# Performance work log

Measured on AMD Instinct MI355X. Metric: run time of the kernel, lower is better.

Reference implementation:

```python
import jax, jax.numpy as jnp
import numpy as np
from jax import lax

B, S, D, V, MAXLEN = 32, 2048, 1024, 32000, 2048
EPS = jnp.finfo(jnp.float32).eps  # torch RMSNorm default eps=None -> finfo eps


def setup_inputs() -> dict:
    key = jax.random.key(0)
    ks = jax.random.split(key, 10)
    w = lambda k, shape: (jax.random.normal(k, shape, jnp.float32) * 0.02)
    return {
        "x": jax.random.randint(ks[0], (B, S), 0, V),
        "emb": w(ks[1], (V, D)),
        "pos": w(ks[2], (MAXLEN, D)),
        "conv_w": w(ks[3], (3, D, D)),            # HIO layout (k, in, out)
        "conv_b": jnp.zeros((D,), jnp.float32),
        "wg1": w(ks[4], (D, D)), "bg1": jnp.zeros((D,), jnp.float32),
        "wmv": w(ks[5], (2 * D, D)), "bmv": jnp.zeros((D,), jnp.float32),
        "wmg": w(ks[6], (2 * D, D)), "bmg": jnp.zeros((D,), jnp.float32),
        "wrg": w(ks[7], (2 * D, D)), "brg": jnp.zeros((D,), jnp.float32),
        "rms_w": jnp.ones((D,), jnp.float32),
        "wp": w(ks[8], (2 * D, V)), "bp": jnp.zeros((V,), jnp.float32),
    }


def _rmsnorm(v, rms_w):
    ms = jnp.mean(v * v, axis=-1, keepdims=True)
    return v * lax.rsqrt(ms + EPS) * rms_w


def reference(x, emb, pos, conv_w, conv_b, wg1, bg1, wmv, bmv, wmg, bmg,
              wrg, brg, rms_w, wp, bp):
    seq_len = x.shape[1]
    h = emb[x] + pos[:seq_len]                     # [B, S, D]
    # Conv1d(D, D, k=3, padding=1) over the sequence axis
    h = lax.conv_general_dilated(h, conv_w, window_strides=(1,),
                                 padding=((1, 1),),
                                 dimension_numbers=("NHC", "HIO", "NHC")) + conv_b
    nodes = h * jax.nn.sigmoid(h @ wg1 + bg1)      # gated nodes [B, S, D]

    curr = nodes[:, :-1, :]                        # nodes_past [B, S-1, D]
    while curr.shape[1] > 1:                       # log2(S) static levels
        if curr.shape[1] % 2 != 0:
            curr = jnp.concatenate([curr, curr[:, -1:, :]], axis=1)
        left = curr[:, 0::2, :]
        right = curr[:, 1::2, :]
        combined = jnp.concatenate([left, right], axis=-1)   # [B, n/2, 2D]
        val = combined @ wmv + bmv
        gate = jax.nn.sigmoid(combined @ wmg + bmg)
        merged = _rmsnorm(val * gate, rms_w)
        res_gate = jax.nn.sigmoid(combined @ wrg + brg)
        residual = (left + right) * 0.5
        curr = res_gate * merged + (1.0 - res_gate) * residual

    root = curr[:, 0, :]                           # [B, D]
    last = nodes[:, -2, :]                         # last of nodes_past
    context = jnp.concatenate([root, last], axis=-1)  # [B, 2D]
    return context @ wp + bp                       # logits [B, V]
```

## Files before the change

### kernel.cpp

```cpp
#include <hip/hip_runtime.h>
#include <stdint.h>

typedef __bf16 bf16_t;
typedef __attribute__((ext_vector_type(8))) __bf16 bf16x8;
typedef __attribute__((ext_vector_type(4))) __bf16 bf16x4;
typedef __attribute__((ext_vector_type(4))) float f32x4;

#define NB 32
#define NS 2048
#define ND 1024
#define NV 32000
#define SP 2050

__device__ __forceinline__ float sigmoid_(float x) { return 1.0f / (1.0f + __expf(-x)); }

__device__ __forceinline__ void gload_lds16(const void* g, void* lds) {
  __builtin_amdgcn_global_load_lds((const __attribute__((address_space(1))) void*)g,
                                   (__attribute__((address_space(3))) void*)lds, 16, 0, 0);
}


__global__ void zero_pad_k(bf16_t* h0p) {
  int i = blockIdx.x;
  int b = i >> 1;
  size_t row = (size_t)b * SP + ((i & 1) ? (SP - 1) : 0);
  bf16x4 z = {};
  *(bf16x4*)(h0p + row * ND + threadIdx.x * 4) = z;
}

__global__ void embed_k(const int* __restrict__ x, const float* __restrict__ emb,
                        const float* __restrict__ pos, bf16_t* __restrict__ h0p) {
  int bs = blockIdx.x;
  int b = bs >> 11, s = bs & (NS - 1);
  int idx = x[bs];
  const float* e = emb + (size_t)idx * ND;
  const float* p = pos + (size_t)s * ND;
  bf16_t* o = h0p + ((size_t)b * SP + s + 1) * ND;
  int d = threadIdx.x * 4;
  f32x4 ev = *(const f32x4*)(e + d);
  f32x4 pv = *(const f32x4*)(p + d);
  bf16x4 ov;
  ov[0] = (bf16_t)(ev[0] + pv[0]);
  ov[1] = (bf16_t)(ev[1] + pv[1]);
  ov[2] = (bf16_t)(ev[2] + pv[2]);
  ov[3] = (bf16_t)(ev[3] + pv[3]);
  *(bf16x4*)(o + d) = ov;
}

__global__ void conv_transpose_k(const float* __restrict__ in, bf16_t* __restrict__ out,
                                 int R, int C) {
  __shared__ float tile[32][33];
  int tc = blockIdx.x * 32, tr = blockIdx.y * 32;
  int tx = threadIdx.x;
  for (int i = threadIdx.y; i < 32; i += 8)
    tile[i][tx] = in[(size_t)(tr + i) * C + tc + tx];
  __syncthreads();
  for (int i = threadIdx.y; i < 32; i += 8)
    out[(size_t)(tc + i) * R + tr + tx] = (bf16_t)tile[tx][i];
}

__global__ void dup_row_k(bf16_t* nodes) {
  int b = blockIdx.x;
  const bf16_t* src = nodes + ((size_t)b * NS + NS - 2) * ND;
  bf16_t* dst = nodes + ((size_t)b * NS + NS - 1) * ND;
  int d = threadIdx.x * 4;
  *(bf16x4*)(dst + d) = *(const bf16x4*)(src + d);
}

__global__ void concat3_k(const float* __restrict__ a, const float* __restrict__ b,
                          const float* __restrict__ c, float* __restrict__ o) {
  int i = blockIdx.x * 256 + threadIdx.x;
  o[i] = i < 1024 ? a[i] : (i < 2048 ? b[i - 1024] : c[i - 2048]);
}

template <int EPI>
__global__ __launch_bounds__(512, 2) void gemm256(
    const bf16_t* __restrict__ A, const bf16_t* __restrict__ Bt,
    const float* __restrict__ bias, const void* aux, void* Cout,
    int M, int N, int K, int lda, int batchShift, int batchPad,
    int GX, int gpx, int nxg, int ych) {
  const int tid = threadIdx.x;
  const int lane = tid & 63;
  const int wave = tid >> 6;
  int n0, m0;
  if (nxg == 0) {
    n0 = (blockIdx.x % GX) * 256;
    m0 = (blockIdx.x / GX) * 256;
  } else {
    const int id = blockIdx.x;
    const int xcd = id & 7;
    const int jb = id >> 3;
    const int xg = xcd % nxg;
    const int ysub = xcd / nxg;
    n0 = (xg * gpx + (jb % gpx)) * 256;
    m0 = (ysub * ych + (jb / gpx)) * 256;
  }
  const int waveM = wave >> 2, waveN = wave & 3;

  __shared__ __align__(16) bf16_t sA[2][256 * 64];
  __shared__ __align__(16) bf16_t sB[2][256 * 64];

  f32x4 acc[8][4] = {};

  const int srow = tid >> 3;
  const int sj = tid & 7;
  const int wbase = wave * 8;

  auto stageA = [&](int buf, int kt, int half) {
#pragma unroll
    for (int r = 0; r < 2; ++r) {
      int lr = half * 128 + r * 64 + srow;
      int sc = sj ^ (lr & 7);
      int g = m0 + lr;
      if (g > M - 1) g = M - 1;
      size_t grow = (size_t)g + (size_t)(((unsigned)g) >> batchShift) * batchPad;
      gload_lds16(A + grow * (size_t)lda + (kt * 64 + sc * 8),
                  &sA[buf][(size_t)(half * 128 + r * 64 + wbase) * 64]);
    }
  };
  auto stageB = [&](int buf, int kt, int half) {
#pragma unroll
    for (int r = 0; r < 2; ++r) {
      int lr = half * 128 + r * 64 + srow;
      int sc = sj ^ (lr & 7);
      int g = n0 + lr;
      if (g > N - 1) g = N - 1;
      gload_lds16(Bt + (size_t)g * K + (kt * 64 + sc * 8),
                  &sB[buf][(size_t)(half * 128 + r * 64 + wbase) * 64]);
    }
  };

  const int nt = K >> 6;
  stageA(0, 0, 0); stageA(0, 0, 1);
  stageB(0, 0, 0); stageB(0, 0, 1);
  if (nt > 1) {
    stageB(1, 1, 0); stageB(1, 1, 1);
    asm volatile("s_waitcnt vmcnt(4)" ::: "memory");
  } else {
    asm volatile("s_waitcnt vmcnt(0)" ::: "memory");
  }
  __builtin_amdgcn_s_barrier();

  const int rlane = lane & 15;
  const int klane = lane >> 4;
  bf16x8 bfr[4][2];

  for (int t = 0; t < nt; ++t) {
    const int buf = t & 1;
    const bf16_t* sa = sA[buf];
    const bf16_t* sb = sB[buf];
#pragma unroll
    for (int p = 0; p < 4; ++p) {
      if (p == 0) {
#pragma unroll
        for (int j = 0; j < 4; ++j)
#pragma unroll
          for (int ks = 0; ks < 2; ++ks) {
            int rb = waveN * 64 + j * 16 + rlane;
            int kc = ks * 4 + klane;
            bfr[j][ks] = *(const bf16x8*)&sb[rb * 64 + ((kc ^ (rb & 7)) * 8)];
          }
      }
      bf16x8 af[2][2];
#pragma unroll
      for (int ii = 0; ii < 2; ++ii)
#pragma unroll
        for (int ks = 0; ks < 2; ++ks) {
          int ra = waveM * 128 + p * 32 + ii * 16 + rlane;
          int kc = ks * 4 + klane;
          af[ii][ks] = *(const bf16x8*)&sa[ra * 64 + ((kc ^ (ra & 7)) * 8)];
        }
      if (p == 0) {
        if (t + 1 < nt) { stageA(buf ^ 1, t + 1, 0); stageA(buf ^ 1, t + 1, 1); }
      } else if (p == 1) {
        if (t + 2 < nt) stageB(buf, t + 2, 0);
      } else if (p == 2) {
        if (t + 2 < nt) stageB(buf, t + 2, 1);
      }
      __builtin_amdgcn_s_barrier();
      __builtin_amdgcn_s_setprio(1);
#pragma unroll
      for (int ks = 0; ks < 2; ++ks)
#pragma unroll
        for (int ii = 0; ii < 2; ++ii)
#pragma unroll
          for (int j = 0; j < 4; ++j)
            acc[p * 2 + ii][j] = __builtin_amdgcn_mfma_f32_16x16x32_bf16(
                af[ii][ks], bfr[j][ks], acc[p * 2 + ii][j], 0, 0, 0);
      __builtin_amdgcn_s_setprio(0);
      if (p < 3) {
        __builtin_amdgcn_s_barrier();
      } else {
        if (t + 2 < nt)
          asm volatile("s_waitcnt vmcnt(4)" ::: "memory");
        else
          asm volatile("s_waitcnt vmcnt(0)" ::: "memory");
        __builtin_amdgcn_s_barrier();
      }
    }
  }

  const int colBase = n0 + waveN * 64 + rlane;
#pragma unroll
  for (int i = 0; i < 8; ++i) {
    const int rowBase = m0 + waveM * 128 + i * 16 + klane * 4;
#pragma unroll
    for (int j = 0; j < 4; ++j) {
      const int col = colBase + j * 16;
      const float bv = bias[col];
#pragma unroll
      for (int r = 0; r < 4; ++r) {
        const int row = rowBase + r;
        if (row >= M) continue;
        float v = acc[i][j][r] + bv;
        size_t o = (size_t)row * N + col;
        if constexpr (EPI == 0) {
          ((bf16_t*)Cout)[o] = (bf16_t)v;
        } else if constexpr (EPI == 1) {
          float hh = (float)((const bf16_t*)aux)[o];
          ((bf16_t*)Cout)[o] = (bf16_t)(hh * sigmoid_(v));
        } else {
          ((bf16_t*)Cout)[o] = (bf16_t)(col < 1024 ? v : sigmoid_(v));
        }
      }
    }
  }
}

template <bool ATOMIC>
__global__ __launch_bounds__(256, 2) void gemm128s(
    const bf16_t* __restrict__ A, const bf16_t* __restrict__ Bt,
    const float* __restrict__ bias, float* __restrict__ Cout,
    int M, int kLen, int nxy) {
  const int tid = threadIdx.x;
  const int lane = tid & 63;
  const int wave = tid >> 6;
  const int id = blockIdx.x;
  const int sk = id / nxy;
  const int rb2 = id % nxy;
  const int n0 = (rb2 % 24) * 128;
  const int m0 = (rb2 / 24) * 128;
  const int kOff = sk * kLen;

  const int waveM = wave >> 1, waveN = wave & 1;

  __shared__ __align__(16) bf16_t sA[2][128 * 64];
  __shared__ __align__(16) bf16_t sB[2][128 * 64];

  f32x4 acc[4][4] = {};

  const int srow = wave * 8 + (lane >> 3);
  const int sj = lane & 7;

  auto stage = [&](int buf, int kk0) {
#pragma unroll
    for (int j = 0; j < 4; ++j) {
      int rowT = j * 32 + srow;
      int k8 = sj ^ (rowT & 7);
      int gm = m0 + rowT;
      if (gm > M - 1) gm = M - 1;
      gload_lds16(A + (size_t)gm * 2048 + (kk0 + k8 * 8), &sA[buf][(j * 256 + wave * 64) * 8]);
      int gn = n0 + rowT;
      gload_lds16(Bt + (size_t)gn * 2048 + (kk0 + k8 * 8), &sB[buf][(j * 256 + wave * 64) * 8]);
    }
  };

  stage(0, kOff);
  __syncthreads();

  const int nt = kLen >> 6;
  int cur = 0;
  const int ar = waveM * 64 + (lane & 15);
  const int br = waveN * 64 + (lane & 15);
  const int kb0 = lane >> 4;

  for (int t = 0; t < nt; ++t) {
    if (t + 1 < nt) stage(cur ^ 1, kOff + (t + 1) * 64);

    const bf16_t* sa = sA[cur];
    const bf16_t* sb = sB[cur];
    bf16x8 af[2][4], bfr[2][4];
#pragma unroll
    for (int ks = 0; ks < 2; ++ks) {
      int kb = kb0 + ks * 4;
#pragma unroll
      for (int i = 0; i < 4; ++i) {
        int ra = ar + i * 16;
        af[ks][i] = *(const bf16x8*)&sa[ra * 64 + ((kb ^ (ra & 7)) * 8)];
        int rbq = br + i * 16;
        bfr[ks][i] = *(const bf16x8*)&sb[rbq * 64 + ((kb ^ (rbq & 7)) * 8)];
      }
    }
#pragma unroll
    for (int ks = 0; ks < 2; ++ks)
#pragma unroll
      for (int i = 0; i < 4; ++i)
#pragma unroll
        for (int j = 0; j < 4; ++j)
          acc[i][j] = __builtin_amdgcn_mfma_f32_16x16x32_bf16(af[ks][i], bfr[ks][j], acc[i][j], 0, 0, 0);
    __syncthreads();
    cur ^= 1;
  }

  const int colBase = n0 + waveN * 64 + (lane & 15);
#pragma unroll
  for (int i = 0; i < 4; ++i) {
    const int rowBase = m0 + waveM * 64 + i * 16 + (lane >> 4) * 4;
#pragma unroll
    for (int jj = 0; jj < 4; ++jj) {
      const int col = colBase + jj * 16;
      const float bv = (!ATOMIC || kOff == 0) ? bias[col] : 0.0f;
#pragma unroll
      for (int r = 0; r < 4; ++r) {
        const int row = rowBase + r;
        if (row >= M) continue;
        float v = acc[i][jj][r] + bv;
        size_t o = (size_t)row * 3072 + col;
        if constexpr (ATOMIC)
          atomicAdd(&Cout[o], v);
        else
          Cout[o] = v;
      }
    }
  }
}

__global__ __launch_bounds__(256) void tree_combine_k(
    const bf16_t* __restrict__ fb, const bf16_t* __restrict__ cur,
    const float* __restrict__ rms_w, bf16_t* __restrict__ outb) {
  const int m = blockIdx.x;
  const int t = threadIdx.x;
  const int d = t * 4;
  const bf16_t* row = fb + (size_t)m * 3072;
  bf16x4 vb = *(const bf16x4*)(row + d);
  bf16x4 gb = *(const bf16x4*)(row + 1024 + d);
  bf16x4 rb = *(const bf16x4*)(row + 2048 + d);
  f32x4 vg;
#pragma unroll
  for (int k = 0; k < 4; ++k) vg[k] = (float)vb[k] * (float)gb[k];
  float ss = vg[0] * vg[0] + vg[1] * vg[1] + vg[2] * vg[2] + vg[3] * vg[3];
#pragma unroll
  for (int o = 32; o > 0; o >>= 1) ss += __shfl_xor(ss, o);
  __shared__ float red[4];
  if ((t & 63) == 0) red[t >> 6] = ss;
  __syncthreads();
  float ms = (red[0] + red[1] + red[2] + red[3]) * (1.0f / ND);
  float scale = rsqrtf(ms + 1.1920929e-07f);
  f32x4 w = *(const f32x4*)(rms_w + d);
  const bf16_t* c0 = cur + (size_t)m * 2048;
  bf16x4 lv = *(const bf16x4*)(c0 + d);
  bf16x4 rv = *(const bf16x4*)(c0 + ND + d);
  bf16x4 o4;
#pragma unroll
  for (int k = 0; k < 4; ++k) {
    float merged = vg[k] * scale * w[k];
    float resid = 0.5f * ((float)lv[k] + (float)rv[k]);
    float g = (float)rb[k];
    o4[k] = (bf16_t)(g * merged + (1.0f - g) * resid);
  }
  *(bf16x4*)(outb + (size_t)m * ND + d) = o4;
}

__global__ __launch_bounds__(256) void tree_combine32_k(
    const float* __restrict__ fb, const bf16_t* __restrict__ cur,
    const float* __restrict__ rms_w, bf16_t* __restrict__ outb) {
  const int m = blockIdx.x;
  const int t = threadIdx.x;
  const int d = t * 4;
  const float* row = fb + (size_t)m * 3072;
  f32x4 v = *(const f32x4*)(row + d);
  f32x4 gl = *(const f32x4*)(row + 1024 + d);
  f32x4 rl = *(const f32x4*)(row + 2048 + d);
  f32x4 vg;
#pragma unroll
  for (int k = 0; k < 4; ++k) vg[k] = v[k] * sigmoid_(gl[k]);
  float ss = vg[0] * vg[0] + vg[1] * vg[1] + vg[2] * vg[2] + vg[3] * vg[3];
#pragma unroll
  for (int o = 32; o > 0; o >>= 1) ss += __shfl_xor(ss, o);
  __shared__ float red[4];
  if ((t & 63) == 0) red[t >> 6] = ss;
  __syncthreads();
  float ms = (red[0] + red[1] + red[2] + red[3]) * (1.0f / ND);
  float scale = rsqrtf(ms + 1.1920929e-07f);
  f32x4 w = *(const f32x4*)(rms_w + d);
  const bf16_t* c0 = cur + (size_t)m * 2048;
  bf16x4 lv = *(const bf16x4*)(c0 + d);
  bf16x4 rv = *(const bf16x4*)(c0 + ND + d);
  bf16x4 o4;
#pragma unroll
  for (int k = 0; k < 4; ++k) {
    float merged = vg[k] * scale * w[k];
    float resid = 0.5f * ((float)lv[k] + (float)rv[k]);
    float g = sigmoid_(rl[k]);
    o4[k] = (bf16_t)(g * merged + (1.0f - g) * resid);
  }
  *(bf16x4*)(outb + (size_t)m * ND + d) = o4;
}

__global__ void build_ctx_k(const bf16_t* __restrict__ root, const bf16_t* __restrict__ nodes,
                            float* __restrict__ ctx) {
  int b = blockIdx.x, t = threadIdx.x;
  const bf16_t* r = root + (size_t)b * ND;
  const bf16_t* l = nodes + ((size_t)b * NS + NS - 2) * ND;
  int d = t * 4;
#pragma unroll
  for (int k = 0; k < 4; ++k) {
    ctx[(size_t)b * 2048 + d + k] = (float)r[d + k];
    ctx[(size_t)b * 2048 + ND + d + k] = (float)l[d + k];
  }
}

__global__ __launch_bounds__(256) void final_proj_k(
    const float* __restrict__ ctx, const float* __restrict__ wp,
    const float* __restrict__ bp, float* __restrict__ out) {
  const int v = blockIdx.x * 256 + threadIdx.x;
  float acc[NB];
#pragma unroll
  for (int b = 0; b < NB; ++b) acc[b] = 0.f;
  __shared__ float sctx[NB][128];
  for (int k0 = 0; k0 < 2048; k0 += 128) {
    __syncthreads();
    for (int i = threadIdx.x; i < NB * 128; i += 256) {
      int bb = i >> 7, kk = i & 127;
      sctx[bb][kk] = ctx[(size_t)bb * 2048 + k0 + kk];
    }
    __syncthreads();
    for (int kk = 0; kk < 128; ++kk) {
      float wv = wp[(size_t)(k0 + kk) * NV + v];
#pragma unroll
      for (int b = 0; b < NB; ++b) acc[b] += sctx[b][kk] * wv;
    }
  }
#pragma unroll
  for (int b = 0; b < NB; ++b) out[(size_t)b * NV + v] = acc[b] + bp[v];
}

extern "C" void kernel_launch(void* const* d_in, const int* in_sizes, int n_in,
                              void* d_out, int out_size, void* d_ws, size_t ws_size,
                              hipStream_t stream) {
  const int* x = (const int*)d_in[0];
  const float* emb = (const float*)d_in[1];
  const float* pos = (const float*)d_in[2];
  const float* conv_w = (const float*)d_in[3];
  const float* conv_b = (const float*)d_in[4];
  const float* wg1 = (const float*)d_in[5];
  const float* bg1 = (const float*)d_in[6];
  const float* wmv = (const float*)d_in[7];
  const float* bmv = (const float*)d_in[8];
  const float* wmg = (const float*)d_in[9];
  const float* bmg = (const float*)d_in[10];
  const float* wrg = (const float*)d_in[11];
  const float* brg = (const float*)d_in[12];
  const float* rms_w = (const float*)d_in[13];
  const float* wp = (const float*)d_in[14];
  const float* bp = (const float*)d_in[15];
  float* out = (float*)d_out;

  char* ws = (char*)d_ws;
  size_t off = 0;
  auto alloc = [&](size_t bytes) -> void* {
    void* p = ws + off;
    off += (bytes + 255) & ~(size_t)255;
    return p;
  };
  bf16_t* h0p = (bf16_t*)alloc((size_t)NB * SP * ND * 2);
  bf16_t* h = (bf16_t*)alloc((size_t)NB * NS * ND * 2);
  bf16_t* nodes = (bf16_t*)alloc((size_t)NB * NS * ND * 2);
  bf16_t* tb0 = (bf16_t*)alloc((size_t)NB * 1024 * ND * 2);
  bf16_t* tb1 = (bf16_t*)alloc((size_t)NB * 1024 * ND * 2);
  bf16_t* convT = (bf16_t*)alloc((size_t)ND * 3072 * 2);
  bf16_t* wg1T = (bf16_t*)alloc((size_t)ND * 1024 * 2);
  bf16_t* wAllT = (bf16_t*)alloc((size_t)3072 * 2048 * 2);
  float* bAll = (float*)alloc((size_t)3072 * 4);
  float* ctx = (float*)alloc((size_t)NB * 2048 * 4);
  if (off > ws_size) return;
  bf16_t* fbuf = (bf16_t*)ws;
  float* fbuf32 = (float*)ws;

  dim3 t256(256), tb32(32, 8);

  conv_transpose_k<<<dim3(ND / 32, 3072 / 32), tb32, 0, stream>>>(conv_w, convT, 3072, ND);
  conv_transpose_k<<<dim3(ND / 32, ND / 32), tb32, 0, stream>>>(wg1, wg1T, ND, ND);
  conv_transpose_k<<<dim3(ND / 32, 2048 / 32), tb32, 0, stream>>>(wmv, wAllT, 2048, ND);
  conv_transpose_k<<<dim3(ND / 32, 2048 / 32), tb32, 0, stream>>>(wmg, wAllT + (size_t)1024 * 2048, 2048, ND);
  conv_transpose_k<<<dim3(ND / 32, 2048 / 32), tb32, 0, stream>>>(wrg, wAllT + (size_t)2048 * 2048, 2048, ND);
  concat3_k<<<12, t256, 0, stream>>>(bmv, bmg, brg, bAll);

  zero_pad_k<<<64, t256, 0, stream>>>(h0p);
  embed_k<<<NB * NS, t256, 0, stream>>>(x, emb, pos, h0p);

  gemm256<0><<<1024, 512, 0, stream>>>(h0p, convT, conv_b, nullptr, h,
                                       NB * NS, ND, 3072, ND, 11, 2, 4, 1, 4, 128);
  gemm256<1><<<1024, 512, 0, stream>>>(h, wg1T, bg1, h, nodes,
                                       NB * NS, ND, ND, ND, 0, 0, 4, 1, 4, 128);
  dup_row_k<<<NB, t256, 0, stream>>>(nodes);

  const bf16_t* cur = nodes;
  bf16_t* bufs[2] = {tb0, tb1};
  int pp = 0;
  for (int L = NS; L > 1; L >>= 1) {
    int M = NB * (L / 2);
    if (M >= 16384) {
      int GY = M / 256;
      gemm256<3><<<12 * GY, 512, 0, stream>>>(cur, wAllT, bAll, nullptr, fbuf,
                                              M, 3072, 2048, 2048, 0, 0, 12, 3, 4, GY / 2);
      tree_combine_k<<<M, t256, 0, stream>>>(fbuf, cur, rms_w, bufs[pp]);
    } else {
      int GY = (M + 127) / 128;
      int nxy = 24 * GY;
      int SK = 1;
      while (nxy * SK < 768 && SK < 16) SK <<= 1;
      if (SK > 1) {
        hipMemsetAsync(fbuf32, 0, (size_t)M * 3072 * 4, stream);
        gemm128s<true><<<nxy * SK, t256, 0, stream>>>(cur, wAllT, bAll, fbuf32,
                                                      M, 2048 / SK, nxy);
      } else {
        gemm128s<false><<<nxy, t256, 0, stream>>>(cur, wAllT, bAll, fbuf32, M, 2048, nxy);
      }
      tree_combine32_k<<<M, t256, 0, stream>>>(fbuf32, cur, rms_w, bufs[pp]);
    }
    cur = bufs[pp];
    pp ^= 1;
  }

  build_ctx_k<<<NB, t256, 0, stream>>>(cur, nodes, ctx);
  final_proj_k<<<NV / 256, t256, 0, stream>>>(ctx, wp, bp, out);
}
```

Baseline: 2.859 ms.

## Restructure GEMM mainloop into 4-stage K=32 ring buffer pipeline

Replaces the double-buffered K=64 tiles with a four-slot ring of K=32 tiles. Each iteration issues a load three steps ahead and then runs all MFMAs for the slot with one barrier, instead of four sub-phases with two barriers each. The aim is fewer barriers per unit of work and deeper prefetch to hide global-load latency. LDS use stays the same. The trade-off is half the MFMA work per barrier and a 4-bank swizzle that may cause more LDS bank conflicts. The loop also assumes nt is a multiple of 4.

Result: no change. 2.819 ms (-1.4%).

```diff
diff --git a/kernel.cpp b/kernel.cpp
--- a/kernel.cpp
+++ b/kernel.cpp
@@ -97,106 +97,74 @@
   }
   const int waveM = wave >> 2, waveN = wave & 3;
 
-  __shared__ __align__(16) bf16_t sA[2][256 * 64];
-  __shared__ __align__(16) bf16_t sB[2][256 * 64];
+  __shared__ __align__(16) bf16_t sA[4][256 * 32];
+  __shared__ __align__(16) bf16_t sB[4][256 * 32];
 
   f32x4 acc[8][4] = {};
 
-  const int srow = tid >> 3;
-  const int sj = tid & 7;
-  const int wbase = wave * 8;
-
-  auto stageA = [&](int buf, int kt, int half) {
+  const int srow = tid >> 2;
+  const int sj = tid & 3;
+  const int wb16 = wave * 16;
+
+  auto stage = [&](int ring, int kt) {
 #pragma unroll
     for (int r = 0; r < 2; ++r) {
-      int lr = half * 128 + r * 64 + srow;
-      int sc = sj ^ (lr & 7);
-      int g = m0 + lr;
-      if (g > M - 1) g = M - 1;
-      size_t grow = (size_t)g + (size_t)(((unsigned)g) >> batchShift) * batchPad;
-      gload_lds16(A + grow * (size_t)lda + (kt * 64 + sc * 8),
-                  &sA[buf][(size_t)(half * 128 + r * 64 + wbase) * 64]);
+      int rowT = r * 128 + srow;
+      int sc = sj ^ (rowT & 3);
+      int gm = m0 + rowT;
+      if (gm > M - 1) gm = M - 1;
+      size_t grow = (size_t)gm + (size_t)(((unsigned)gm) >> batchShift) * batchPad;
+      gload_lds16(A + grow * (size_t)lda + (kt * 32 + sc * 8),
+                  &sA[ring][(size_t)(r * 128 + wb16) * 32]);
+      int gn = n0 + rowT;
+      if (gn > N - 1) gn = N - 1;
+      gload_lds16(Bt + (size_t)gn * K + (kt * 32 + sc * 8),
+                  &sB[ring][(size_t)(r * 128 + wb16) * 32]);
     }
   };
-  auto stageB = [&](int buf, int kt, int half) {
-#pragma unroll
-    for (int r = 0; r < 2; ++r) {
-      int lr = half * 128 + r * 64 + srow;
-      int sc = sj ^ (lr & 7);
-      int g = n0 + lr;
-      if (g > N - 1) g = N - 1;
-      gload_lds16(Bt + (size_t)g * K + (kt * 64 + sc * 8),
-                  &sB[buf][(size_t)(half * 128 + r * 64 + wbase) * 64]);
-    }
-  };
-
-  const int nt = K >> 6;
-  stageA(0, 0, 0); stageA(0, 0, 1);
-  stageB(0, 0, 0); stageB(0, 0, 1);
-  if (nt > 1) {
-    stageB(1, 1, 0); stageB(1, 1, 1);
-    asm volatile("s_waitcnt vmcnt(4)" ::: "memory");
-  } else {
-    asm volatile("s_waitcnt vmcnt(0)" ::: "memory");
-  }
+
+  const int nt = K >> 5;
+  stage(0, 0);
+  stage(1, 1);
+  stage(2, 2);
+  asm volatile("s_waitcnt vmcnt(8)" ::: "memory");
   __builtin_amdgcn_s_barrier();
+  __builtin_amdgcn_sched_barrier(0);
 
   const int rlane = lane & 15;
   const int klane = lane >> 4;
-  bf16x8 bfr[4][2];
-
-  for (int t = 0; t < nt; ++t) {
-    const int buf = t & 1;
-    const bf16_t* sa = sA[buf];
-    const bf16_t* sb = sB[buf];
-#pragma unroll
-    for (int p = 0; p < 4; ++p) {
-      if (p == 0) {
+
+  for (int t0 = 0; t0 < nt; t0 += 4) {
+#pragma unroll
+    for (int u = 0; u < 4; ++u) {
+      const int t = t0 + u;
+      if (t + 3 < nt) stage((u + 3) & 3, t + 3);
+      const bf16_t* sa = sA[u];
+      const bf16_t* sb = sB[u];
+      bf16x8 af[8], bfr[4];
+#pragma unroll
+      for (int j = 0; j < 4; ++j) {
+        int rb = waveN * 64 + j * 16 + rlane;
+        bfr[j] = *(const bf16x8*)&sb[rb * 32 + ((klane ^ (rb & 3)) * 8)];
+      }
+#pragma unroll
+      for (int i = 0; i < 8; ++i) {
+        int ra = waveM * 128 + i * 16 + rlane;
+        af[i] = *(const bf16x8*)&sa[ra * 32 + ((klane ^ (ra & 3)) * 8)];
+      }
+      __builtin_amdgcn_s_setprio(1);
+#pragma unroll
+      for (int i = 0; i < 8; ++i)
 #pragma unroll
         for (int j = 0; j < 4; ++j)
-#pragma unroll
-          for (int ks = 0; ks < 2; ++ks) {
-            int rb = waveN * 64 + j * 16 + rlane;
-            int kc = ks * 4 + klane;
-            bfr[j][ks] = *(const bf16x8*)&sb[rb * 64 + ((kc ^ (rb & 7)) * 8)];
-          }
-      }
-      bf16x8 af[2][2];
-#pragma unroll
-      for (int ii = 0; ii < 2; ++ii)
-#pragma unroll
-        for (int ks = 0; ks < 2; ++ks) {
-          int ra = waveM * 128 + p * 32 + ii * 16 + rlane;
-          int kc = ks * 4 + klane;
-          af[ii][ks] = *(const bf16x8*)&sa[ra * 64 + ((kc ^ (ra & 7)) * 8)];
-        }
-      if (p == 0) {
-        if (t + 1 < nt) { stageA(buf ^ 1, t + 1, 0); stageA(buf ^ 1, t + 1, 1); }
-      } else if (p == 1) {
-        if (t + 2 < nt) stageB(buf, t + 2, 0);
-      } else if (p == 2) {
-        if (t + 2 < nt) stageB(buf, t + 2, 1);
-      }
+          acc[i][j] = __builtin_amdgcn_mfma_f32_16x16x32_bf16(af[i], bfr[j], acc[i][j], 0, 0, 0);
+      __builtin_amdgcn_s_setprio(0);
+      if (t + 3 < nt)
+        asm volatile("s_waitcnt vmcnt(8)" ::: "memory");
+      else
+        asm volatile("s_waitcnt vmcnt(0)" ::: "memory");
       __builtin_amdgcn_s_barrier();
-      __builtin_amdgcn_s_setprio(1);
-#pragma unroll
-      for (int ks = 0; ks < 2; ++ks)
-#pragma unroll
-        for (int ii = 0; ii < 2; ++ii)
-#pragma unroll
-          for (int j = 0; j < 4; ++j)
-            acc[p * 2 + ii][j] = __builtin_amdgcn_mfma_f32_16x16x32_bf16(
-                af[ii][ks], bfr[j][ks], acc[p * 2 + ii][j], 0, 0, 0);
-      __builtin_amdgcn_s_setprio(0);
-      if (p < 3) {
-        __builtin_amdgcn_s_barrier();
-      } else {
-        if (t + 2 < nt)
-          asm volatile("s_waitcnt vmcnt(4)" ::: "memory");
-        else
-          asm volatile("s_waitcnt vmcnt(0)" ::: "memory");
-        __builtin_amdgcn_s_barrier();
-      }
+      __builtin_amdgcn_sched_barrier(0);
     }
   }
 
```
